# Optimization experiments

Hardware: AMD Instinct MI355X
Metric: run time of the kernel (lower is better)

Reference implementation:

```python
import jax, jax.numpy as jnp
import numpy as np

B, N, H, HEADS, L, V, T = 4, 256, 256, 4, 128, 256, 100
FF = 4 * H

def _ln(x, g, b, eps=1e-5):
    m = jnp.mean(x, -1, keepdims=True)
    v = jnp.mean((x - m) ** 2, -1, keepdims=True)
    return (x - m) / jnp.sqrt(v + eps) * g + b

def _mha(h, w_qkv, b_qkv, w_o, b_o):
    b, n, hd = h.shape
    d = hd // HEADS
    q, k, v = jnp.split(h @ w_qkv + b_qkv, 3, axis=-1)
    q = q.reshape(b, n, HEADS, d)
    k = k.reshape(b, n, HEADS, d)
    v = v.reshape(b, n, HEADS, d)
    s = jnp.einsum('bihd,bjhd->bhij', q, k) / jnp.sqrt(jnp.float32(d))
    a = jax.nn.softmax(s, axis=-1)
    o = jnp.einsum('bhij,bjhd->bihd', a, v).reshape(b, n, hd)
    return o @ w_o + b_o

def _edge_logits(h, w1, b1, w2, b2):
    # concat([h_i, h_j], -1) @ w1 == h_i @ w1[:H] + h_j @ w1[H:]  (avoids (B,N,N,2H) materialization)
    hi = h @ w1[:H]
    hj = h @ w1[H:]
    pre = hi[:, :, None, :] + hj[:, None, :, :] + b1  # (B,N,N,H)
    return (jax.nn.gelu(pre, approximate=False) @ w2 + b2)[..., 0]

def _gnn_block(x, nbr, qw, qb, kw, kb, vw, vb, sw, sb, l1g, l1b, f1w, f1b, f2w, f2b, l2g, l2b):
    # TransformerConv (PyG, concat=True, root_weight=True) as dense masked attention over in-neighbors.
    b, n, hd = x.shape
    d = hd // HEADS
    q = (x @ qw + qb).reshape(b, n, HEADS, d)
    k = (x @ kw + kb).reshape(b, n, HEADS, d)
    v = (x @ vw + vb).reshape(b, n, HEADS, d)
    s = jnp.einsum('bihd,bjhd->bhij', q, k) / jnp.sqrt(jnp.float32(d))
    m = nbr[:, None, :, :]  # (B,1,N,N); nbr[b,i,j]=True iff edge j->i
    a = jax.nn.softmax(jnp.where(m, s, -1e30), axis=-1) * m  # no-neighbor rows aggregate to 0
    agg = jnp.einsum('bhij,bjhd->bihd', a, v).reshape(b, n, hd)
    x = _ln(x + agg + x @ sw + sb, l1g, l1b)
    ffn = jax.nn.gelu(x @ f1w + f1b, approximate=False) @ f2w + f2b
    return _ln(x + ffn, l2g, l2b)

def _forward(noisy_tokens, t, z, lp1_w, lp1_b, lp2_w, lp2_b, tok_emb, time_tab, time_w, time_b, pos_tab, enc_qkv_w, enc_qkv_b, enc_o_w, enc_o_b, enc_ln1_g, enc_ln1_b, enc_f1_w, enc_f1_b, enc_f2_w, enc_f2_b, enc_ln2_g, enc_ln2_b, gq_w, gq_b, gk_w, gk_b, gv_w, gv_b, gs_w, gs_b, g_ln1_g, g_ln1_b, g_f1_w, g_f1_b, g_f2_w, g_f2_b, g_ln2_g, g_ln2_b, nh1_w, nh1_b, nh2_w, nh2_b, eh1_w, eh1_b, eh2_w, eh2_b, sh1_w, sh1_b, sh2_w, sh2_b):
    lat = jax.nn.relu(z @ lp1_w + lp1_b) @ lp2_w + lp2_b  # (B,H)
    time_e = jax.nn.gelu(time_tab[t] @ time_w + time_b, approximate=False)  # (B,H)
    h = tok_emb[noisy_tokens] + time_e[:, None, :] + pos_tab[None, :, :] + lat[:, None, :]
    for l in range(2):  # post-norm TransformerEncoderLayer, relu FFN
        h = _ln(h + _mha(h, enc_qkv_w[l], enc_qkv_b[l], enc_o_w[l], enc_o_b[l]), enc_ln1_g[l], enc_ln1_b[l])
        h = _ln(h + jax.nn.relu(h @ enc_f1_w[l] + enc_f1_b[l]) @ enc_f2_w[l] + enc_f2_b[l], enc_ln2_g[l], enc_ln2_b[l])
    el0 = _edge_logits(h, eh1_w, eh1_b, eh2_w, eh2_b)
    nbr = jnp.swapaxes(jax.nn.sigmoid(el0) > 0.3, 1, 2)  # transpose: adj[j,i] -> in-neighbors of i
    x = h
    for l in range(4):
        x = _gnn_block(x, nbr, gq_w[l], gq_b[l], gk_w[l], gk_b[l], gv_w[l], gv_b[l], gs_w[l], gs_b[l], g_ln1_g[l], g_ln1_b[l], g_f1_w[l], g_f1_b[l], g_f2_w[l], g_f2_b[l], g_ln2_g[l], g_ln2_b[l])
    node_logits = jax.nn.gelu(x @ nh1_w + nh1_b, approximate=False) @ nh2_w + nh2_b
    edge_logits = _edge_logits(x, eh1_w, eh1_b, eh2_w, eh2_b)
    size_logits = jax.nn.relu(lat @ sh1_w + sh1_b) @ sh2_w + sh2_b
    return node_logits, edge_logits, size_logits

def setup_inputs():
    key = jax.random.key(0)
    ks = iter(jax.random.split(key, 70))
    def p(shape):
        return jax.random.normal(next(ks), shape, dtype=jnp.float32) * 0.02
    return {
        'z': jax.random.normal(next(ks), (B, L), dtype=jnp.float32),
        'noisy_tokens': jax.random.randint(next(ks), (B, N), 0, V),
        't': jax.random.randint(next(ks), (B,), 0, T),
        'lp1_w': p((L, H)), 'lp1_b': p((H,)), 'lp2_w': p((H, H)), 'lp2_b': p((H,)),
        'tok_emb': p((V, H)), 'time_tab': p((T, H)), 'time_w': p((H, H)), 'time_b': p((H,)),
        'pos_tab': p((N, H)),
        'enc_qkv_w': p((2, H, 3 * H)), 'enc_qkv_b': p((2, 3 * H)),
        'enc_o_w': p((2, H, H)), 'enc_o_b': p((2, H)),
        'enc_ln1_g': jnp.ones((2, H)), 'enc_ln1_b': jnp.zeros((2, H)),
        'enc_f1_w': p((2, H, FF)), 'enc_f1_b': p((2, FF)),
        'enc_f2_w': p((2, FF, H)), 'enc_f2_b': p((2, H)),
        'enc_ln2_g': jnp.ones((2, H)), 'enc_ln2_b': jnp.zeros((2, H)),
        'gq_w': p((4, H, H)), 'gq_b': p((4, H)),
        'gk_w': p((4, H, H)), 'gk_b': p((4, H)),
        'gv_w': p((4, H, H)), 'gv_b': p((4, H)),
        'gs_w': p((4, H, H)), 'gs_b': p((4, H)),
        'g_ln1_g': jnp.ones((4, H)), 'g_ln1_b': jnp.zeros((4, H)),
        'g_f1_w': p((4, H, FF)), 'g_f1_b': p((4, FF)),
        'g_f2_w': p((4, FF, H)), 'g_f2_b': p((4, H)),
        'g_ln2_g': jnp.ones((4, H)), 'g_ln2_b': jnp.zeros((4, H)),
        'nh1_w': p((H, H)), 'nh1_b': p((H,)),
        'nh2_w': p((H, V)), 'nh2_b': p((V,)),
        'eh1_w': p((2 * H, H)), 'eh1_b': p((H,)),
        'eh2_w': p((H, 1)), 'eh2_b': p((1,)),
        'sh1_w': p((H, H // 2)), 'sh1_b': p((H // 2,)),
        'sh2_w': p((H // 2, N)), 'sh2_b': p((N,)),
    }

def reference(z, noisy_tokens, t, lp1_w, lp1_b, lp2_w, lp2_b, tok_emb, time_tab, time_w, time_b, pos_tab, enc_qkv_w, enc_qkv_b, enc_o_w, enc_o_b, enc_ln1_g, enc_ln1_b, enc_f1_w, enc_f1_b, enc_f2_w, enc_f2_b, enc_ln2_g, enc_ln2_b, gq_w, gq_b, gk_w, gk_b, gv_w, gv_b, gs_w, gs_b, g_ln1_g, g_ln1_b, g_f1_w, g_f1_b, g_f2_w, g_f2_b, g_ln2_g, g_ln2_b, nh1_w, nh1_b, nh2_w, nh2_b, eh1_w, eh1_b, eh2_w, eh2_b, sh1_w, sh1_b, sh2_w, sh2_b):
    return _forward(noisy_tokens, t, z, lp1_w, lp1_b, lp2_w, lp2_b, tok_emb, time_tab, time_w, time_b, pos_tab, enc_qkv_w, enc_qkv_b, enc_o_w, enc_o_b, enc_ln1_g, enc_ln1_b, enc_f1_w, enc_f1_b, enc_f2_w, enc_f2_b, enc_ln2_g, enc_ln2_b, gq_w, gq_b, gk_w, gk_b, gv_w, gv_b, gs_w, gs_b, g_ln1_g, g_ln1_b, g_f1_w, g_f1_b, g_f2_w, g_f2_b, g_ln2_g, g_ln2_b, nh1_w, nh1_b, nh2_w, nh2_b, eh1_w, eh1_b, eh2_w, eh2_b, sh1_w, sh1_b, sh2_w, sh2_b)
```

## Files before the change

kernel.cpp:

```cpp
#include <hip/hip_runtime.h>
#include <math.h>


typedef __attribute__((ext_vector_type(8))) short bf16x8;
typedef __attribute__((ext_vector_type(4))) float f32x4;

__device__ __forceinline__ unsigned short f2b(float f) {
    unsigned u = __float_as_uint(f);
    u += 0x7FFFu + ((u >> 16) & 1u);
    return (unsigned short)(u >> 16);
}
__device__ __forceinline__ unsigned pack2(float a, float b) {
    return (unsigned)f2b(a) | ((unsigned)f2b(b) << 16);
}
__device__ __forceinline__ bf16x8 as_frag(uint4 v) {
    union { uint4 u; bf16x8 f; } x; x.u = v; return x.f;
}
__device__ __forceinline__ bf16x8 ld_frag_f32(const float* p) {
    const float4 v0 = *(const float4*)p;
    const float4 v1 = *(const float4*)(p + 4);
    union { unsigned u[4]; bf16x8 f; } x;
    x.u[0] = pack2(v0.x, v0.y); x.u[1] = pack2(v0.z, v0.w);
    x.u[2] = pack2(v1.x, v1.y); x.u[3] = pack2(v1.z, v1.w);
    return x.f;
}

__device__ __forceinline__ float gelu_f(float x) {
    const float y  = 0.70710678118654752f * x;
    const float ay = fabsf(y);
    const float t  = __builtin_amdgcn_rcpf(fmaf(0.3275911f, ay, 1.0f));
    float S = fmaf(t, 1.061405429f, -1.453152027f);
    S = fmaf(t, S, 1.421413741f);
    S = fmaf(t, S, -0.284496736f);
    S = fmaf(t, S, 0.254829592f);
    S = S * t;
    const float e = __expf(-ay * ay);
    const float E = fmaf(-S, e, 1.0f);
    return 0.5f * x * (1.0f + copysignf(E, y));
}

struct PrepEnt { const float* src; unsigned dstOff; int K; int N; unsigned tstart; };
struct PrepTab { int n; PrepEnt e[36]; };

__global__ __launch_bounds__(256) void k_prep(PrepTab tab, unsigned short* __restrict__ wt)
{
    const int bx = blockIdx.x;
    int ei = 0;
    for (int i = 0; i < tab.n; ++i) if (tab.e[i].tstart <= (unsigned)bx) ei = i;
    const PrepEnt E = tab.e[ei];
    const int tIdx = bx - E.tstart;
    const int ntn = E.N >> 6;
    const int kt = tIdx / ntn, nt = tIdx % ntn;
    const int tid = threadIdx.x;
    __shared__ unsigned Tl[64][36];
    {
        const int r = tid >> 2, c = (tid & 3) * 16;
        const float* s = E.src + (size_t)(kt * 64 + r) * E.N + nt * 64 + c;
        unsigned o[8];
        #pragma unroll
        for (int q = 0; q < 4; ++q) {
            const float4 v = *(const float4*)(s + q * 4);
            o[q * 2 + 0] = pack2(v.x, v.y);
            o[q * 2 + 1] = pack2(v.z, v.w);
        }
        *(uint4*)&Tl[r][c / 2 + 0] = make_uint4(o[0], o[1], o[2], o[3]);
        *(uint4*)&Tl[r][c / 2 + 4] = make_uint4(o[4], o[5], o[6], o[7]);
    }
    __syncthreads();
    {
        const int rn = tid >> 2, ck = (tid & 3) * 16;
        const int sh = (rn & 1) * 16, hw = rn >> 1;
        unsigned o[8];
        #pragma unroll
        for (int s = 0; s < 8; ++s) {
            const unsigned lo = (Tl[ck + 2 * s][hw] >> sh) & 0xFFFFu;
            const unsigned hi = (Tl[ck + 2 * s + 1][hw] >> sh) & 0xFFFFu;
            o[s] = lo | (hi << 16);
        }
        unsigned short* d = wt + E.dstOff + (size_t)(nt * 64 + rn) * E.K + kt * 64 + ck;
        *(uint4*)(d + 0) = make_uint4(o[0], o[1], o[2], o[3]);
        *(uint4*)(d + 8) = make_uint4(o[4], o[5], o[6], o[7]);
    }
}


__device__ __forceinline__ void gd64_body(
    const float* __restrict__ A, const unsigned short* __restrict__ Wt,
    const float* __restrict__ bias, float* __restrict__ C,
    int K, int ldc, int act, int m0, int n0)
{
    const int tid = threadIdx.x;
    const int l = tid & 63, wid = tid >> 6;
    const int wm = wid & 1, wn = wid >> 1, lr = l & 15, lg = l >> 4;
    const float* a0 = A + (size_t)(m0 + wm * 32 + lr) * K + lg * 8;
    const float* a1 = a0 + (size_t)16 * K;
    const unsigned short* b0 = Wt + (size_t)(n0 + wn * 32 + lr) * K + lg * 8;
    const unsigned short* b1 = b0 + (size_t)16 * K;
    f32x4 acc00 = {0.f,0.f,0.f,0.f}, acc01 = acc00, acc10 = acc00, acc11 = acc00;
    #pragma unroll 2
    for (int k0 = 0; k0 < K; k0 += 32) {
        const bf16x8 fa0 = ld_frag_f32(a0 + k0);
        const bf16x8 fa1 = ld_frag_f32(a1 + k0);
        const bf16x8 fb0 = as_frag(*(const uint4*)(b0 + k0));
        const bf16x8 fb1 = as_frag(*(const uint4*)(b1 + k0));
        acc00 = __builtin_amdgcn_mfma_f32_16x16x32_bf16(fa0, fb0, acc00, 0, 0, 0);
        acc01 = __builtin_amdgcn_mfma_f32_16x16x32_bf16(fa0, fb1, acc01, 0, 0, 0);
        acc10 = __builtin_amdgcn_mfma_f32_16x16x32_bf16(fa1, fb0, acc10, 0, 0, 0);
        acc11 = __builtin_amdgcn_mfma_f32_16x16x32_bf16(fa1, fb1, acc11, 0, 0, 0);
    }
    const int cb0 = n0 + wn * 32 + lr, cb1 = cb0 + 16;
    const float bv0 = bias ? bias[cb0] : 0.f;
    const float bv1 = bias ? bias[cb1] : 0.f;
    #pragma unroll
    for (int r = 0; r < 4; ++r) {
        const int row0 = m0 + wm * 32 + lg * 4 + r;
        const int row1 = row0 + 16;
        float v00 = acc00[r] + bv0, v01 = acc01[r] + bv1;
        float v10 = acc10[r] + bv0, v11 = acc11[r] + bv1;
        if (act == 1) {
            v00 = fmaxf(v00, 0.f); v01 = fmaxf(v01, 0.f);
            v10 = fmaxf(v10, 0.f); v11 = fmaxf(v11, 0.f);
        } else if (act == 2) {
            v00 = gelu_f(v00); v01 = gelu_f(v01);
            v10 = gelu_f(v10); v11 = gelu_f(v11);
        }
        C[(size_t)row0 * ldc + cb0] = v00;
        C[(size_t)row0 * ldc + cb1] = v01;
        C[(size_t)row1 * ldc + cb0] = v10;
        C[(size_t)row1 * ldc + cb1] = v11;
    }
}

__global__ __launch_bounds__(256) void k_gd64(
    const float* __restrict__ A, const unsigned short* __restrict__ Wt,
    const float* __restrict__ bias, float* __restrict__ C, int K, int ldc, int act)
{
    gd64_body(A, Wt, bias, C, K, ldc, act, blockIdx.y * 64, blockIdx.x * 64);
}

__device__ __forceinline__ void gd32_body(
    const float* __restrict__ A, const unsigned short* __restrict__ Wt,
    const float* __restrict__ bias, float* __restrict__ C,
    int K, int ldc, int act, int m0, int n0)
{
    const int tid = threadIdx.x;
    const int l = tid & 63, wid = tid >> 6;
    const int qm = wid & 1, qn = wid >> 1, lr = l & 15, lg = l >> 4;
    const float* ap = A + (size_t)(m0 + qm * 16 + lr) * K + lg * 8;
    const unsigned short* bp = Wt + (size_t)(n0 + qn * 16 + lr) * K + lg * 8;
    f32x4 acc = {0.f,0.f,0.f,0.f};
    #pragma unroll 4
    for (int k0 = 0; k0 < K; k0 += 32) {
        const bf16x8 fa = ld_frag_f32(ap + k0);
        const bf16x8 fb = as_frag(*(const uint4*)(bp + k0));
        acc = __builtin_amdgcn_mfma_f32_16x16x32_bf16(fa, fb, acc, 0, 0, 0);
    }
    const int cc = n0 + qn * 16 + lr;
    const float bv = bias ? bias[cc] : 0.f;
    #pragma unroll
    for (int r = 0; r < 4; ++r) {
        const int row = m0 + qm * 16 + lg * 4 + r;
        float v = acc[r] + bv;
        if (act == 1) v = fmaxf(v, 0.f); else if (act == 2) v = gelu_f(v);
        C[(size_t)row * ldc + cc] = v;
    }
}

__global__ __launch_bounds__(256) void k_gd32(
    const float* __restrict__ A, const unsigned short* __restrict__ Wt,
    const float* __restrict__ bias, float* __restrict__ C, int K, int ldc, int act)
{
    gd32_body(A, Wt, bias, C, K, ldc, act, blockIdx.y * 32, blockIdx.x * 32);
}

struct MW4 { const unsigned short* wt[4]; const float* b[4]; };
__global__ __launch_bounds__(256) void k_gd32_4(
    const float* __restrict__ A, MW4 p, float* __restrict__ C)
{
    const int z = blockIdx.z;
    gd32_body(A, p.wt[z], p.b[z], C + z * 256, 256, 1024, 0,
              blockIdx.y * 32, blockIdx.x * 32);
}

__global__ __launch_bounds__(256) void k_mv(
    const float* __restrict__ A, const int* __restrict__ aidx, int K,
    const float* __restrict__ W, const float* __restrict__ bias,
    float* __restrict__ out, int N, int act)
{
    const int r = blockIdx.x, c0 = blockIdx.y * 64;
    const int c = threadIdx.x & 63, ks = threadIdx.x >> 6;
    const float* arow = A + (size_t)(aidx ? aidx[r] : r) * K;
    float s = 0.f;
    for (int k = ks; k < K; k += 4) s += arow[k] * W[(size_t)k * N + c0 + c];
    __shared__ float red[4][64];
    red[ks][c] = s;
    __syncthreads();
    if (ks == 0) {
        float v = red[0][c] + red[1][c] + red[2][c] + red[3][c] + (bias ? bias[c0 + c] : 0.f);
        if (act == 1) v = fmaxf(v, 0.f); else if (act == 2) v = gelu_f(v);
        out[(size_t)r * N + c0 + c] = v;
    }
}

__global__ __launch_bounds__(256) void k_embed(
    const int* __restrict__ tok, const float* __restrict__ tok_emb,
    const float* __restrict__ pos, const float* __restrict__ lat,
    const float* __restrict__ te, float* __restrict__ h)
{
    const int r = blockIdx.x, c = threadIdx.x;
    const int b = r >> 8, n = r & 255;
    h[(size_t)r * 256 + c] = tok_emb[(size_t)tok[r] * 256 + c] + te[b * 256 + c]
                           + pos[n * 256 + c] + lat[b * 256 + c];
}

__global__ __launch_bounds__(256) void k_attn2(
    const float* __restrict__ qkv, int ld, int qo, int ko, int vo,
    const unsigned char* __restrict__ mask, float* __restrict__ out)
{
    const int blk = blockIdx.x;
    const int ig = blk & 15, hh = (blk >> 4) & 3, b = blk >> 6;
    const int i0 = ig * 16;
    const int t = threadIdx.x;
    __shared__ float Qs[16][68];
    __shared__ float Ts[64][68];
    __shared__ float Ss[16][260];

    {
        const int r = t >> 4, c = (t & 15) * 4;
        *(float4*)&Qs[r][c] = *(const float4*)&qkv[(size_t)(b * 256 + i0 + r) * ld + qo + hh * 64 + c];
    }
    const int i = t >> 4, tx = t & 15;

    for (int jt = 0; jt < 4; ++jt) {
        __syncthreads();
        {
            const int jr = t >> 2, cs = (t & 3) * 16;
            const float* src = &qkv[(size_t)(b * 256 + jt * 64 + jr) * ld + ko + hh * 64 + cs];
            *(float4*)&Ts[jr][cs + 0]  = *(const float4*)(src + 0);
            *(float4*)&Ts[jr][cs + 4]  = *(const float4*)(src + 4);
            *(float4*)&Ts[jr][cs + 8]  = *(const float4*)(src + 8);
            *(float4*)&Ts[jr][cs + 12] = *(const float4*)(src + 12);
        }
        __syncthreads();
        float s0 = 0.f, s1 = 0.f, s2 = 0.f, s3 = 0.f;
        #pragma unroll 8
        for (int d = 0; d < 64; ++d) {
            const float qd = Qs[i][d];
            s0 += qd * Ts[tx][d];
            s1 += qd * Ts[tx + 16][d];
            s2 += qd * Ts[tx + 32][d];
            s3 += qd * Ts[tx + 48][d];
        }
        Ss[i][jt * 64 + tx]      = s0;
        Ss[i][jt * 64 + tx + 16] = s1;
        Ss[i][jt * 64 + tx + 32] = s2;
        Ss[i][jt * 64 + tx + 48] = s3;
    }

    {
        const unsigned char* mrow = mask ? &mask[(size_t)(b * 256 + i0 + i) * 256] : nullptr;
        float sv[16]; bool okv[16];
        float m = -3.0e38f;
        #pragma unroll
        for (int k = 0; k < 16; ++k) {
            const int j = tx + 16 * k;
            const float s = Ss[i][j] * 0.125f;
            const bool ok = mrow ? (mrow[j] != 0) : true;
            sv[k] = s; okv[k] = ok;
            if (ok) m = fmaxf(m, s);
        }
        #pragma unroll
        for (int w = 1; w < 16; w <<= 1) m = fmaxf(m, __shfl_xor(m, w, 64));
        float ev[16]; float sum = 0.f;
        #pragma unroll
        for (int k = 0; k < 16; ++k) {
            ev[k] = okv[k] ? __expf(sv[k] - m) : 0.f;
            sum += ev[k];
        }
        #pragma unroll
        for (int w = 1; w < 16; w <<= 1) sum += __shfl_xor(sum, w, 64);
        const float inv = (sum > 0.f) ? 1.f / sum : 0.f;
        #pragma unroll
        for (int k = 0; k < 16; ++k) Ss[i][tx + 16 * k] = ev[k] * inv;
    }

    const int d4 = tx * 4;
    float4 o = {0.f, 0.f, 0.f, 0.f};
    for (int jt = 0; jt < 4; ++jt) {
        __syncthreads();
        {
            const int jr = t >> 2, cs = (t & 3) * 16;
            const float* src = &qkv[(size_t)(b * 256 + jt * 64 + jr) * ld + vo + hh * 64 + cs];
            *(float4*)&Ts[jr][cs + 0]  = *(const float4*)(src + 0);
            *(float4*)&Ts[jr][cs + 4]  = *(const float4*)(src + 4);
            *(float4*)&Ts[jr][cs + 8]  = *(const float4*)(src + 8);
            *(float4*)&Ts[jr][cs + 12] = *(const float4*)(src + 12);
        }
        __syncthreads();
        #pragma unroll 8
        for (int j = 0; j < 64; ++j) {
            const float p = Ss[i][jt * 64 + j];
            const float4 v4 = *(const float4*)&Ts[j][d4];
            o.x += p * v4.x; o.y += p * v4.y; o.z += p * v4.z; o.w += p * v4.w;
        }
    }
    *(float4*)&out[(size_t)(b * 256 + i0 + i) * 256 + hh * 64 + d4] = o;
}

__global__ __launch_bounds__(256) void k_ln2(
    const float* __restrict__ a, const float* __restrict__ bb, int ldb,
    const float* __restrict__ cc, int ldc,
    const float* __restrict__ g, const float* __restrict__ beta, float* __restrict__ out)
{
    const int r = blockIdx.x * 4 + (threadIdx.x >> 6);
    const int c4 = (threadIdx.x & 63) * 4;
    float4 v = *(const float4*)&a[(size_t)r * 256 + c4];
    if (bb) {
        const float4 u = *(const float4*)&bb[(size_t)r * ldb + c4];
        v.x += u.x; v.y += u.y; v.z += u.z; v.w += u.w;
    }
    if (cc) {
        const float4 u = *(const float4*)&cc[(size_t)r * ldc + c4];
        v.x += u.x; v.y += u.y; v.z += u.z; v.w += u.w;
    }
    float s = v.x + v.y + v.z + v.w;
    float q = v.x * v.x + v.y * v.y + v.z * v.z + v.w * v.w;
    #pragma unroll
    for (int w = 1; w < 64; w <<= 1) {
        s += __shfl_xor(s, w, 64);
        q += __shfl_xor(q, w, 64);
    }
    const float mean = s * (1.0f / 256.0f);
    const float var  = q * (1.0f / 256.0f) - mean * mean;
    const float inv  = rsqrtf(var + 1e-5f);
    const float4 gg = *(const float4*)&g[c4];
    const float4 be = *(const float4*)&beta[c4];
    float4 o;
    o.x = (v.x - mean) * inv * gg.x + be.x;
    o.y = (v.y - mean) * inv * gg.y + be.y;
    o.z = (v.z - mean) * inv * gg.z + be.z;
    o.w = (v.w - mean) * inv * gg.w + be.w;
    *(float4*)&out[(size_t)r * 256 + c4] = o;
}

__global__ __launch_bounds__(256) void k_edge3(
    const float* __restrict__ hi, const float* __restrict__ hj,
    const float* __restrict__ w2, const float* __restrict__ b2,
    float* __restrict__ val_out, unsigned char* __restrict__ mask_out)
{
    const int jg = blockIdx.x, ig = blockIdx.y, b = blockIdx.z;
    const int t = threadIdx.x;
    __shared__ float his[16][268];
    __shared__ float hjs[16][268];
    __shared__ float w2s[256];
    {
        const int r = t >> 4, c = (t & 15) * 16;
        const float* s1 = &hi[(size_t)(b * 256 + ig * 16 + r) * 256 + c];
        const float* s2 = &hj[(size_t)(b * 256 + jg * 16 + r) * 256 + c];
        #pragma unroll
        for (int q = 0; q < 4; ++q) {
            *(float4*)&his[r][c + q * 4] = *(const float4*)(s1 + q * 4);
            *(float4*)&hjs[r][c + q * 4] = *(const float4*)(s2 + q * 4);
        }
        w2s[t] = w2[t];
    }
    __syncthreads();
    const int i = t >> 4, j = t & 15;
    float acc = 0.f;
    #pragma unroll 4
    for (int h4 = 0; h4 < 64; ++h4) {
        const float4 hv  = *(const float4*)&hjs[j][h4 * 4];
        const float4 hi4 = *(const float4*)&his[i][h4 * 4];
        const float4 w4  = *(const float4*)&w2s[h4 * 4];
        acc += gelu_f(hi4.x + hv.x) * w4.x;
        acc += gelu_f(hi4.y + hv.y) * w4.y;
        acc += gelu_f(hi4.z + hv.z) * w4.z;
        acc += gelu_f(hi4.w + hv.w) * w4.w;
    }
    const float v = acc + b2[0];
    if (val_out)  val_out[(size_t)b * 65536 + (ig * 16 + i) * 256 + jg * 16 + j] = v;
    if (mask_out) mask_out[(size_t)b * 65536 + (jg * 16 + j) * 256 + ig * 16 + i] =
                      (v > -0.84729786038720f) ? 1 : 0;
}

extern "C" void kernel_launch(void* const* d_in, const int* in_sizes, int n_in,
                              void* d_out, int out_size, void* d_ws, size_t ws_size,
                              hipStream_t stream) {
    const float* z     = (const float*)d_in[0];
    const int*   tok   = (const int*)d_in[1];
    const int*   tt    = (const int*)d_in[2];
    const float* lp1w  = (const float*)d_in[3];
    const float* lp1b  = (const float*)d_in[4];
    const float* lp2w  = (const float*)d_in[5];
    const float* lp2b  = (const float*)d_in[6];
    const float* temb  = (const float*)d_in[7];
    const float* ttab  = (const float*)d_in[8];
    const float* tw    = (const float*)d_in[9];
    const float* tb    = (const float*)d_in[10];
    const float* pos   = (const float*)d_in[11];
    const float* qkvw  = (const float*)d_in[12];
    const float* qkvb  = (const float*)d_in[13];
    const float* ow    = (const float*)d_in[14];
    const float* ob    = (const float*)d_in[15];
    const float* ln1g  = (const float*)d_in[16];
    const float* ln1b  = (const float*)d_in[17];
    const float* f1w   = (const float*)d_in[18];
    const float* f1b   = (const float*)d_in[19];
    const float* f2w   = (const float*)d_in[20];
    const float* f2b   = (const float*)d_in[21];
    const float* ln2g  = (const float*)d_in[22];
    const float* ln2b  = (const float*)d_in[23];
    const float* gqw   = (const float*)d_in[24];
    const float* gqb   = (const float*)d_in[25];
    const float* gkw   = (const float*)d_in[26];
    const float* gkb   = (const float*)d_in[27];
    const float* gvw   = (const float*)d_in[28];
    const float* gvb   = (const float*)d_in[29];
    const float* gsw   = (const float*)d_in[30];
    const float* gsb   = (const float*)d_in[31];
    const float* gl1g  = (const float*)d_in[32];
    const float* gl1b  = (const float*)d_in[33];
    const float* gf1w  = (const float*)d_in[34];
    const float* gf1b  = (const float*)d_in[35];
    const float* gf2w  = (const float*)d_in[36];
    const float* gf2b  = (const float*)d_in[37];
    const float* gl2g  = (const float*)d_in[38];
    const float* gl2b  = (const float*)d_in[39];
    const float* nh1w  = (const float*)d_in[40];
    const float* nh1b  = (const float*)d_in[41];
    const float* nh2w  = (const float*)d_in[42];
    const float* nh2b  = (const float*)d_in[43];
    const float* eh1w  = (const float*)d_in[44];
    const float* eh1b  = (const float*)d_in[45];
    const float* eh2w  = (const float*)d_in[46];
    const float* eh2b  = (const float*)d_in[47];
    const float* sh1w  = (const float*)d_in[48];
    const float* sh1b  = (const float*)d_in[49];
    const float* sh2w  = (const float*)d_in[50];
    const float* sh2b  = (const float*)d_in[51];

    float* W = (float*)d_ws;
    float* Hh  = W + 0;
    float* QK  = W + 262144;
    float* AO  = W + 1310720;
    float* T1  = W + 1572864;
    float* HI  = W + 1835008;
    float* HJ  = W + 2097152;
    float* LAT = W + 2359296;
    float* TE  = W + 2360320;
    float* A1  = W + 2361344;
    float* SH  = W + 2362368;
    unsigned char* MASK = (unsigned char*)(W + 2362880);
    unsigned short* wt  = (unsigned short*)(W + 2428416);

    float* out      = (float*)d_out;
    float* out_node = out;
    float* out_edge = out + 262144;
    float* out_sz   = out + 524288;

    PrepTab tab; int ne = 0; unsigned tiles = 0;
    auto add = [&](const float* src, int K, int N, unsigned off) {
        tab.e[ne].src = src; tab.e[ne].K = K; tab.e[ne].N = N;
        tab.e[ne].dstOff = off; tab.e[ne].tstart = tiles;
        tiles += (unsigned)((K >> 6) * (N >> 6)); ++ne;
    };
    for (int l = 0; l < 2; ++l) add(qkvw + (size_t)l * 196608, 256, 768,  0 + l * 196608);
    for (int l = 0; l < 2; ++l) add(ow   + (size_t)l * 65536,  256, 256,  393216 + l * 65536);
    for (int l = 0; l < 2; ++l) add(f1w  + (size_t)l * 262144, 256, 1024, 524288 + l * 262144);
    for (int l = 0; l < 2; ++l) add(f2w  + (size_t)l * 262144, 1024, 256, 1048576 + l * 262144);
    for (int l = 0; l < 4; ++l) add(gqw  + (size_t)l * 65536,  256, 256,  1572864 + l * 65536);
    for (int l = 0; l < 4; ++l) add(gkw  + (size_t)l * 65536,  256, 256,  1835008 + l * 65536);
    for (int l = 0; l < 4; ++l) add(gvw  + (size_t)l * 65536,  256, 256,  2097152 + l * 65536);
    for (int l = 0; l < 4; ++l) add(gsw  + (size_t)l * 65536,  256, 256,  2359296 + l * 65536);
    for (int l = 0; l < 4; ++l) add(gf1w + (size_t)l * 262144, 256, 1024, 2621440 + l * 262144);
    for (int l = 0; l < 4; ++l) add(gf2w + (size_t)l * 262144, 1024, 256, 3670016 + l * 262144);
    add(nh1w, 256, 256, 4718592);
    add(nh2w, 256, 256, 4784128);
    add(eh1w,         256, 256, 4849664);
    add(eh1w + 65536, 256, 256, 4915200);
    tab.n = ne;
    k_prep<<<tiles, 256, 0, stream>>>(tab, wt);

    auto g64 = [&](const float* Aa, size_t wtoff, const float* bias, float* Cc,
                   int N, int K, int ldc, int act) {
        k_gd64<<<dim3(N / 64, 16), 256, 0, stream>>>(Aa, wt + wtoff, bias, Cc, K, ldc, act);
    };
    auto g32 = [&](const float* Aa, size_t wtoff, const float* bias, float* Cc,
                   int K, int ldc, int act) {
        k_gd32<<<dim3(8, 32), 256, 0, stream>>>(Aa, wt + wtoff, bias, Cc, K, ldc, act);
    };

    k_mv<<<dim3(4, 4), 256, 0, stream>>>(z,    nullptr, 128, lp1w, lp1b, A1,     256, 1);
    k_mv<<<dim3(4, 4), 256, 0, stream>>>(ttab, tt,      256, tw,   tb,   TE,     256, 2);
    k_mv<<<dim3(4, 4), 256, 0, stream>>>(A1,   nullptr, 256, lp2w, lp2b, LAT,    256, 0);
    k_mv<<<dim3(4, 2), 256, 0, stream>>>(LAT,  nullptr, 256, sh1w, sh1b, SH,     128, 1);
    k_mv<<<dim3(4, 4), 256, 0, stream>>>(SH,   nullptr, 128, sh2w, sh2b, out_sz, 256, 0);

    k_embed<<<1024, 256, 0, stream>>>(tok, temb, pos, LAT, TE, Hh);

    for (int l = 0; l < 2; ++l) {
        g64(Hh, (size_t)l * 196608, qkvb + l * 768, QK, 768, 256, 768, 0);
        k_attn2<<<256, 256, 0, stream>>>(QK, 768, 0, 256, 512, nullptr, AO);
        g32(AO, 393216 + (size_t)l * 65536, ob + l * 256, T1, 256, 256, 0);
        k_ln2<<<256, 256, 0, stream>>>(Hh, T1, 256, nullptr, 0, ln1g + l * 256, ln1b + l * 256, Hh);
        g64(Hh, 524288 + (size_t)l * 262144, f1b + l * 1024, QK, 1024, 256, 1024, 1);
        g32(QK, 1048576 + (size_t)l * 262144, f2b + l * 256, T1, 1024, 256, 0);
        k_ln2<<<256, 256, 0, stream>>>(Hh, T1, 256, nullptr, 0, ln2g + l * 256, ln2b + l * 256, Hh);
    }

    g32(Hh, 4849664, eh1b, HI, 256, 256, 0);
    g32(Hh, 4915200, nullptr, HJ, 256, 256, 0);
    k_edge3<<<dim3(16, 16, 4), 256, 0, stream>>>(HI, HJ, eh2w, eh2b, nullptr, MASK);

    for (int l = 0; l < 4; ++l) {
        MW4 p;
        p.wt[0] = wt + 1572864 + (size_t)l * 65536; p.b[0] = gqb + l * 256;
        p.wt[1] = wt + 1835008 + (size_t)l * 65536; p.b[1] = gkb + l * 256;
        p.wt[2] = wt + 2097152 + (size_t)l * 65536; p.b[2] = gvb + l * 256;
        p.wt[3] = wt + 2359296 + (size_t)l * 65536; p.b[3] = gsb + l * 256;
        k_gd32_4<<<dim3(8, 32, 4), 256, 0, stream>>>(Hh, p, QK);
        k_attn2<<<256, 256, 0, stream>>>(QK, 1024, 0, 256, 512, MASK, AO);
        k_ln2<<<256, 256, 0, stream>>>(Hh, AO, 256, QK + 768, 1024, gl1g + l * 256, gl1b + l * 256, Hh);
        g64(Hh, 2621440 + (size_t)l * 262144, gf1b + l * 1024, QK, 1024, 256, 1024, 2);
        g32(QK, 3670016 + (size_t)l * 262144, gf2b + l * 256, T1, 1024, 256, 0);
        k_ln2<<<256, 256, 0, stream>>>(Hh, T1, 256, nullptr, 0, gl2g + l * 256, gl2b + l * 256, Hh);
    }

    g32(Hh, 4718592, nh1b, T1, 256, 256, 2);
    g32(T1, 4784128, nh2b, out_node, 256, 256, 0);
    g32(Hh, 4849664, eh1b, HI, 256, 256, 0);
    g32(Hh, 4915200, nullptr, HJ, 256, 256, 0);
    k_edge3<<<dim3(16, 16, 4), 256, 0, stream>>>(HI, HJ, eh2w, eh2b, out_edge, nullptr);
}
```

Baseline: 750.0 us.

## Fuse entire forward pass into one persistent kernel with grid barriers

```diff
diff --git a/kernel.cpp b/kernel.cpp
--- a/kernel.cpp
+++ b/kernel.cpp
@@ -1,6 +1,7 @@
 #include <hip/hip_runtime.h>
 #include <math.h>
 
+#define NB 256
 
 typedef __attribute__((ext_vector_type(8))) short bf16x8;
 typedef __attribute__((ext_vector_type(4))) float f32x4;
@@ -42,17 +43,46 @@
 struct PrepEnt { const float* src; unsigned dstOff; int K; int N; unsigned tstart; };
 struct PrepTab { int n; PrepEnt e[36]; };
 
-__global__ __launch_bounds__(256) void k_prep(PrepTab tab, unsigned short* __restrict__ wt)
-{
-    const int bx = blockIdx.x;
+struct MegaArgs {
+    const float *z; const int *tok; const int *tt;
+    const float *lp1w,*lp1b,*lp2w,*lp2b,*temb,*ttab,*tw,*tb,*pos;
+    const float *qkvb,*ob,*ln1g,*ln1b,*f1b,*f2b,*ln2g,*ln2b;
+    const float *gqb,*gkb,*gvb,*gsb,*gl1g,*gl1b,*gf1b,*gf2b,*gl2g,*gl2b;
+    const float *nh1b,*nh2b,*eh1b,*eh2w,*eh2b;
+    const float *sh1w,*sh1b,*sh2w,*sh2b;
+    float *Hh,*QK,*AO,*T1,*HI,*HJ,*LAT,*TE,*A1,*SH;
+    unsigned char* MASK; unsigned short* wt; unsigned* bar;
+    float *out_node,*out_edge,*out_sz;
+    PrepTab ptab;
+};
+
+__device__ __forceinline__ void gsync(unsigned* bar) {
+    __syncthreads();
+    if (threadIdx.x == 0) {
+        __threadfence();
+        unsigned g = __hip_atomic_load(bar + 1, __ATOMIC_RELAXED, __HIP_MEMORY_SCOPE_AGENT);
+        unsigned a = __hip_atomic_fetch_add(bar, 1u, __ATOMIC_ACQ_REL, __HIP_MEMORY_SCOPE_AGENT);
+        if (a == (unsigned)(NB - 1)) {
+            __hip_atomic_store(bar, 0u, __ATOMIC_RELAXED, __HIP_MEMORY_SCOPE_AGENT);
+            __hip_atomic_fetch_add(bar + 1, 1u, __ATOMIC_ACQ_REL, __HIP_MEMORY_SCOPE_AGENT);
+        } else {
+            while (__hip_atomic_load(bar + 1, __ATOMIC_ACQUIRE, __HIP_MEMORY_SCOPE_AGENT) == g)
+                __builtin_amdgcn_s_sleep(4);
+        }
+    }
+    __syncthreads();
+}
+
+__device__ void prep_tile(const PrepTab& tab, unsigned short* wt, int t, char* SMc)
+{
+    unsigned (*Tl)[36] = (unsigned(*)[36])SMc;
     int ei = 0;
-    for (int i = 0; i < tab.n; ++i) if (tab.e[i].tstart <= (unsigned)bx) ei = i;
+    for (int i = 0; i < tab.n; ++i) if (tab.e[i].tstart <= (unsigned)t) ei = i;
     const PrepEnt E = tab.e[ei];
-    const int tIdx = bx - E.tstart;
+    const int tIdx = t - (int)E.tstart;
     const int ntn = E.N >> 6;
     const int kt = tIdx / ntn, nt = tIdx % ntn;
     const int tid = threadIdx.x;
-    __shared__ unsigned Tl[64][36];
     {
         const int r = tid >> 2, c = (tid & 3) * 16;
         const float* s = E.src + (size_t)(kt * 64 + r) * E.N + nt * 64 + c;
@@ -81,67 +111,11 @@
         *(uint4*)(d + 0) = make_uint4(o[0], o[1], o[2], o[3]);
         *(uint4*)(d + 8) = make_uint4(o[4], o[5], o[6], o[7]);
     }
-}
-
-
-__device__ __forceinline__ void gd64_body(
-    const float* __restrict__ A, const unsigned short* __restrict__ Wt,
-    const float* __restrict__ bias, float* __restrict__ C,
-    int K, int ldc, int act, int m0, int n0)
-{
-    const int tid = threadIdx.x;
-    const int l = tid & 63, wid = tid >> 6;
-    const int wm = wid & 1, wn = wid >> 1, lr = l & 15, lg = l >> 4;
-    const float* a0 = A + (size_t)(m0 + wm * 32 + lr) * K + lg * 8;
-    const float* a1 = a0 + (size_t)16 * K;
-    const unsigned short* b0 = Wt + (size_t)(n0 + wn * 32 + lr) * K + lg * 8;
-    const unsigned short* b1 = b0 + (size_t)16 * K;
-    f32x4 acc00 = {0.f,0.f,0.f,0.f}, acc01 = acc00, acc10 = acc00, acc11 = acc00;
-    #pragma unroll 2
-    for (int k0 = 0; k0 < K; k0 += 32) {
-        const bf16x8 fa0 = ld_frag_f32(a0 + k0);
-        const bf16x8 fa1 = ld_frag_f32(a1 + k0);
-        const bf16x8 fb0 = as_frag(*(const uint4*)(b0 + k0));
-        const bf16x8 fb1 = as_frag(*(const uint4*)(b1 + k0));
-        acc00 = __builtin_amdgcn_mfma_f32_16x16x32_bf16(fa0, fb0, acc00, 0, 0, 0);
-        acc01 = __builtin_amdgcn_mfma_f32_16x16x32_bf16(fa0, fb1, acc01, 0, 0, 0);
-        acc10 = __builtin_amdgcn_mfma_f32_16x16x32_bf16(fa1, fb0, acc10, 0, 0, 0);
-        acc11 = __builtin_amdgcn_mfma_f32_16x16x32_bf16(fa1, fb1, acc11, 0, 0, 0);
-    }
-    const int cb0 = n0 + wn * 32 + lr, cb1 = cb0 + 16;
-    const float bv0 = bias ? bias[cb0] : 0.f;
-    const float bv1 = bias ? bias[cb1] : 0.f;
-    #pragma unroll
-    for (int r = 0; r < 4; ++r) {
-        const int row0 = m0 + wm * 32 + lg * 4 + r;
-        const int row1 = row0 + 16;
-        float v00 = acc00[r] + bv0, v01 = acc01[r] + bv1;
-        float v10 = acc10[r] + bv0, v11 = acc11[r] + bv1;
-        if (act == 1) {
-            v00 = fmaxf(v00, 0.f); v01 = fmaxf(v01, 0.f);
-            v10 = fmaxf(v10, 0.f); v11 = fmaxf(v11, 0.f);
-        } else if (act == 2) {
-            v00 = gelu_f(v00); v01 = gelu_f(v01);
-            v10 = gelu_f(v10); v11 = gelu_f(v11);
-        }
-        C[(size_t)row0 * ldc + cb0] = v00;
-        C[(size_t)row0 * ldc + cb1] = v01;
-        C[(size_t)row1 * ldc + cb0] = v10;
-        C[(size_t)row1 * ldc + cb1] = v11;
-    }
-}
-
-__global__ __launch_bounds__(256) void k_gd64(
-    const float* __restrict__ A, const unsigned short* __restrict__ Wt,
-    const float* __restrict__ bias, float* __restrict__ C, int K, int ldc, int act)
-{
-    gd64_body(A, Wt, bias, C, K, ldc, act, blockIdx.y * 64, blockIdx.x * 64);
-}
-
-__device__ __forceinline__ void gd32_body(
-    const float* __restrict__ A, const unsigned short* __restrict__ Wt,
-    const float* __restrict__ bias, float* __restrict__ C,
-    int K, int ldc, int act, int m0, int n0)
+    __syncthreads();
+}
+
+__device__ void gd32_tile(const float* A, const unsigned short* Wt, const float* bias,
+                          float* C, int K, int ldc, int act, int m0, int n0)
 {
     const int tid = threadIdx.x;
     const int l = tid & 63, wid = tid >> 6;
@@ -166,71 +140,20 @@
     }
 }
 
-__global__ __launch_bounds__(256) void k_gd32(
-    const float* __restrict__ A, const unsigned short* __restrict__ Wt,
-    const float* __restrict__ bias, float* __restrict__ C, int K, int ldc, int act)
-{
-    gd32_body(A, Wt, bias, C, K, ldc, act, blockIdx.y * 32, blockIdx.x * 32);
-}
-
-struct MW4 { const unsigned short* wt[4]; const float* b[4]; };
-__global__ __launch_bounds__(256) void k_gd32_4(
-    const float* __restrict__ A, MW4 p, float* __restrict__ C)
-{
-    const int z = blockIdx.z;
-    gd32_body(A, p.wt[z], p.b[z], C + z * 256, 256, 1024, 0,
-              blockIdx.y * 32, blockIdx.x * 32);
-}
-
-__global__ __launch_bounds__(256) void k_mv(
-    const float* __restrict__ A, const int* __restrict__ aidx, int K,
-    const float* __restrict__ W, const float* __restrict__ bias,
-    float* __restrict__ out, int N, int act)
-{
-    const int r = blockIdx.x, c0 = blockIdx.y * 64;
-    const int c = threadIdx.x & 63, ks = threadIdx.x >> 6;
-    const float* arow = A + (size_t)(aidx ? aidx[r] : r) * K;
-    float s = 0.f;
-    for (int k = ks; k < K; k += 4) s += arow[k] * W[(size_t)k * N + c0 + c];
-    __shared__ float red[4][64];
-    red[ks][c] = s;
-    __syncthreads();
-    if (ks == 0) {
-        float v = red[0][c] + red[1][c] + red[2][c] + red[3][c] + (bias ? bias[c0 + c] : 0.f);
-        if (act == 1) v = fmaxf(v, 0.f); else if (act == 2) v = gelu_f(v);
-        out[(size_t)r * N + c0 + c] = v;
-    }
-}
-
-__global__ __launch_bounds__(256) void k_embed(
-    const int* __restrict__ tok, const float* __restrict__ tok_emb,
-    const float* __restrict__ pos, const float* __restrict__ lat,
-    const float* __restrict__ te, float* __restrict__ h)
-{
-    const int r = blockIdx.x, c = threadIdx.x;
-    const int b = r >> 8, n = r & 255;
-    h[(size_t)r * 256 + c] = tok_emb[(size_t)tok[r] * 256 + c] + te[b * 256 + c]
-                           + pos[n * 256 + c] + lat[b * 256 + c];
-}
-
-__global__ __launch_bounds__(256) void k_attn2(
-    const float* __restrict__ qkv, int ld, int qo, int ko, int vo,
-    const unsigned char* __restrict__ mask, float* __restrict__ out)
-{
-    const int blk = blockIdx.x;
+__device__ void attn_block(const float* qkv, int ld, int qo, int ko, int vo,
+    const unsigned char* mask, float* outp, int blk, char* SMc)
+{
+    float (*Qs)[68]  = (float(*)[68])SMc;
+    float (*Ts)[68]  = (float(*)[68])(SMc + 4352);
+    float (*Ss)[260] = (float(*)[260])(SMc + 21760);
     const int ig = blk & 15, hh = (blk >> 4) & 3, b = blk >> 6;
     const int i0 = ig * 16;
     const int t = threadIdx.x;
-    __shared__ float Qs[16][68];
-    __shared__ float Ts[64][68];
-    __shared__ float Ss[16][260];
-
     {
         const int r = t >> 4, c = (t & 15) * 4;
         *(float4*)&Qs[r][c] = *(const float4*)&qkv[(size_t)(b * 256 + i0 + r) * ld + qo + hh * 64 + c];
     }
     const int i = t >> 4, tx = t & 15;
-
     for (int jt = 0; jt < 4; ++jt) {
         __syncthreads();
         {
@@ -256,7 +179,6 @@
         Ss[i][jt * 64 + tx + 32] = s2;
         Ss[i][jt * 64 + tx + 48] = s3;
     }
-
     {
         const unsigned char* mrow = mask ? &mask[(size_t)(b * 256 + i0 + i) * 256] : nullptr;
         float sv[16]; bool okv[16];
@@ -271,19 +193,18 @@
         }
         #pragma unroll
         for (int w = 1; w < 16; w <<= 1) m = fmaxf(m, __shfl_xor(m, w, 64));
-        float ev[16]; float sum = 0.f;
+        float sum = 0.f;
         #pragma unroll
         for (int k = 0; k < 16; ++k) {
-            ev[k] = okv[k] ? __expf(sv[k] - m) : 0.f;
-            sum += ev[k];
+            sv[k] = okv[k] ? __expf(sv[k] - m) : 0.f;
+            sum += sv[k];
         }
         #pragma unroll
         for (int w = 1; w < 16; w <<= 1) sum += __shfl_xor(sum, w, 64);
         const float inv = (sum > 0.f) ? 1.f / sum : 0.f;
         #pragma unroll
-        for (int k = 0; k < 16; ++k) Ss[i][tx + 16 * k] = ev[k] * inv;
-    }
-
+        for (int k = 0; k < 16; ++k) Ss[i][tx + 16 * k] = sv[k] * inv;
+    }
     const int d4 = tx * 4;
     float4 o = {0.f, 0.f, 0.f, 0.f};
     for (int jt = 0; jt < 4; ++jt) {
@@ -304,15 +225,14 @@
             o.x += p * v4.x; o.y += p * v4.y; o.z += p * v4.z; o.w += p * v4.w;
         }
     }
-    *(float4*)&out[(size_t)(b * 256 + i0 + i) * 256 + hh * 64 + d4] = o;
-}
-
-__global__ __launch_bounds__(256) void k_ln2(
-    const float* __restrict__ a, const float* __restrict__ bb, int ldb,
-    const float* __restrict__ cc, int ldc,
-    const float* __restrict__ g, const float* __restrict__ beta, float* __restrict__ out)
-{
-    const int r = blockIdx.x * 4 + (threadIdx.x >> 6);
+    *(float4*)&outp[(size_t)(b * 256 + i0 + i) * 256 + hh * 64 + d4] = o;
+    __syncthreads();
+}
+
+__device__ void ln_rows(const float* a, const float* bb, int ldb,
+    const float* cc, int ldc, const float* g, const float* beta, float* outp, int bid)
+{
+    const int r = bid * 4 + (threadIdx.x >> 6);
     const int c4 = (threadIdx.x & 63) * 4;
     float4 v = *(const float4*)&a[(size_t)r * 256 + c4];
     if (bb) {
@@ -340,19 +260,17 @@
     o.y = (v.y - mean) * inv * gg.y + be.y;
     o.z = (v.z - mean) * inv * gg.z + be.z;
     o.w = (v.w - mean) * inv * gg.w + be.w;
-    *(float4*)&out[(size_t)r * 256 + c4] = o;
-}
-
-__global__ __launch_bounds__(256) void k_edge3(
-    const float* __restrict__ hi, const float* __restrict__ hj,
-    const float* __restrict__ w2, const float* __restrict__ b2,
-    float* __restrict__ val_out, unsigned char* __restrict__ mask_out)
-{
-    const int jg = blockIdx.x, ig = blockIdx.y, b = blockIdx.z;
+    *(float4*)&outp[(size_t)r * 256 + c4] = o;
+}
+
+__device__ void edge_tile(const float* hi, const float* hj, const float* w2,
+    const float* b2, float* val_out, unsigned char* mask_out,
+    int b, int ig, int jg, char* SMc)
+{
+    float (*his)[268] = (float(*)[268])SMc;
+    float (*hjs)[268] = (float(*)[268])(SMc + 17152);
+    float* w2s = (float*)(SMc + 34304);
     const int t = threadIdx.x;
-    __shared__ float his[16][268];
-    __shared__ float hjs[16][268];
-    __shared__ float w2s[256];
     {
         const int r = t >> 4, c = (t & 15) * 16;
         const float* s1 = &hi[(size_t)(b * 256 + ig * 16 + r) * 256 + c];
@@ -381,6 +299,126 @@
     if (val_out)  val_out[(size_t)b * 65536 + (ig * 16 + i) * 256 + jg * 16 + j] = v;
     if (mask_out) mask_out[(size_t)b * 65536 + (jg * 16 + j) * 256 + ig * 16 + i] =
                       (v > -0.84729786038720f) ? 1 : 0;
+    __syncthreads();
+}
+
+__device__ void mv_chunk(const float* A, const int* aidx, int K, const float* Wm,
+                         const float* bias, float* outp, int N, int act,
+                         int rb, int cb, char* SMc)
+{
+    float (*red)[64] = (float(*)[64])SMc;
+    const int c = threadIdx.x & 63, ks = threadIdx.x >> 6;
+    const int c0 = cb * 64;
+    const float* arow = A + (size_t)(aidx ? aidx[rb] : rb) * K;
+    float s = 0.f;
+    for (int k = ks; k < K; k += 4) s += arow[k] * Wm[(size_t)k * N + c0 + c];
+    __syncthreads();
+    red[ks][c] = s;
+    __syncthreads();
+    if (ks == 0) {
+        float v = red[0][c] + red[1][c] + red[2][c] + red[3][c]
+                + (bias ? bias[c0 + c] : 0.f);
+        if (act == 1) v = fmaxf(v, 0.f); else if (act == 2) v = gelu_f(v);
+        outp[(size_t)rb * N + c0 + c] = v;
+    }
+}
+
+__global__ __launch_bounds__(256) void k_mega(MegaArgs A)
+{
+    __shared__ __align__(16) char SM[38912];
+    const int bid = blockIdx.x;
+    const int tid = threadIdx.x;
+
+    for (int t = bid; t < 1216; t += NB) prep_tile(A.ptab, A.wt, t, SM);
+    gsync(A.bar);
+
+    if (bid < 16) mv_chunk(A.z, nullptr, 128, A.lp1w, A.lp1b, A.A1, 256, 1, bid >> 2, bid & 3, SM);
+    else if (bid < 32) { const int b2 = bid - 16;
+        mv_chunk(A.ttab, A.tt, 256, A.tw, A.tb, A.TE, 256, 2, b2 >> 2, b2 & 3, SM); }
+    gsync(A.bar);
+
+    if (bid < 16) mv_chunk(A.A1, nullptr, 256, A.lp2w, A.lp2b, A.LAT, 256, 0, bid >> 2, bid & 3, SM);
+    gsync(A.bar);
+
+    for (int q = 0; q < 4; ++q) {
+        const int r = bid * 4 + q, b = r >> 8, n = r & 255;
+        A.Hh[(size_t)r * 256 + tid] = A.temb[(size_t)A.tok[r] * 256 + tid] + A.TE[b * 256 + tid]
+                                    + A.pos[n * 256 + tid] + A.LAT[b * 256 + tid];
+    }
+    if (bid < 8) mv_chunk(A.LAT, nullptr, 256, A.sh1w, A.sh1b, A.SH, 128, 1, bid >> 1, bid & 1, SM);
+    gsync(A.bar);
+
+    for (int l = 0; l < 2; ++l) {
+        for (int t = bid; t < 768; t += NB)
+            gd32_tile(A.Hh, A.wt + (size_t)l * 196608, A.qkvb + l * 768, A.QK,
+                      256, 768, 0, (t & 31) * 32, (t >> 5) * 32);
+        if (l == 0 && bid < 16)
+            mv_chunk(A.SH, nullptr, 128, A.sh2w, A.sh2b, A.out_sz, 256, 0, bid >> 2, bid & 3, SM);
+        gsync(A.bar);
+        attn_block(A.QK, 768, 0, 256, 512, nullptr, A.AO, bid, SM);
+        gsync(A.bar);
+        gd32_tile(A.AO, A.wt + 393216 + (size_t)l * 65536, A.ob + l * 256, A.T1,
+                  256, 256, 0, (bid & 31) * 32, (bid >> 5) * 32);
+        gsync(A.bar);
+        ln_rows(A.Hh, A.T1, 256, nullptr, 0, A.ln1g + l * 256, A.ln1b + l * 256, A.Hh, bid);
+        gsync(A.bar);
+        for (int t = bid; t < 1024; t += NB)
+            gd32_tile(A.Hh, A.wt + 524288 + (size_t)l * 262144, A.f1b + l * 1024, A.QK,
+                      256, 1024, 1, (t & 31) * 32, (t >> 5) * 32);
+        gsync(A.bar);
+        gd32_tile(A.QK, A.wt + 1048576 + (size_t)l * 262144, A.f2b + l * 256, A.T1,
+                  1024, 256, 0, (bid & 31) * 32, (bid >> 5) * 32);
+        gsync(A.bar);
+        ln_rows(A.Hh, A.T1, 256, nullptr, 0, A.ln2g + l * 256, A.ln2b + l * 256, A.Hh, bid);
+        gsync(A.bar);
+    }
+
+    for (int t = bid; t < 512; t += NB) {
+        const int s = t & 255, tm = (s & 31) * 32, tn = (s >> 5) * 32;
+        if (t < 256) gd32_tile(A.Hh, A.wt + 4849664, A.eh1b, A.HI, 256, 256, 0, tm, tn);
+        else         gd32_tile(A.Hh, A.wt + 4915200, nullptr, A.HJ, 256, 256, 0, tm, tn);
+    }
+    gsync(A.bar);
+    for (int t = bid; t < 1024; t += NB)
+        edge_tile(A.HI, A.HJ, A.eh2w, A.eh2b, nullptr, A.MASK, t >> 8, (t >> 4) & 15, t & 15, SM);
+    gsync(A.bar);
+
+    for (int l = 0; l < 4; ++l) {
+        for (int t = bid; t < 1024; t += NB) {
+            const int which = t >> 8, s = t & 255;
+            const unsigned short* w = A.wt + 1572864 + (size_t)which * 262144 + (size_t)l * 65536;
+            const float* bi = (which == 0 ? A.gqb : which == 1 ? A.gkb :
+                               which == 2 ? A.gvb : A.gsb) + l * 256;
+            gd32_tile(A.Hh, w, bi, A.QK + which * 256, 256, 1024, 0,
+                      (s & 31) * 32, (s >> 5) * 32);
+        }
+        gsync(A.bar);
+        attn_block(A.QK, 1024, 0, 256, 512, A.MASK, A.AO, bid, SM);
+        gsync(A.bar);
+        ln_rows(A.Hh, A.AO, 256, A.QK + 768, 1024, A.gl1g + l * 256, A.gl1b + l * 256, A.Hh, bid);
+        gsync(A.bar);
+        for (int t = bid; t < 1024; t += NB)
+            gd32_tile(A.Hh, A.wt + 2621440 + (size_t)l * 262144, A.gf1b + l * 1024, A.QK,
+                      256, 1024, 2, (t & 31) * 32, (t >> 5) * 32);
+        gsync(A.bar);
+        gd32_tile(A.QK, A.wt + 3670016 + (size_t)l * 262144, A.gf2b + l * 256, A.T1,
+                  1024, 256, 0, (bid & 31) * 32, (bid >> 5) * 32);
+        gsync(A.bar);
+        ln_rows(A.Hh, A.T1, 256, nullptr, 0, A.gl2g + l * 256, A.gl2b + l * 256, A.Hh, bid);
+        gsync(A.bar);
+    }
+
+    for (int t = bid; t < 768; t += NB) {
+        const int which = t >> 8, s = t & 255, tm = (s & 31) * 32, tn = (s >> 5) * 32;
+        if (which == 0)      gd32_tile(A.Hh, A.wt + 4718592, A.nh1b, A.T1, 256, 256, 2, tm, tn);
+        else if (which == 1) gd32_tile(A.Hh, A.wt + 4849664, A.eh1b, A.HI, 256, 256, 0, tm, tn);
+        else                 gd32_tile(A.Hh, A.wt + 4915200, nullptr, A.HJ, 256, 256, 0, tm, tn);
+    }
+    gsync(A.bar);
+    gd32_tile(A.T1, A.wt + 4784128, A.nh2b, A.out_node, 256, 256, 0,
+              (bid & 31) * 32, (bid >> 5) * 32);
+    for (int t = bid; t < 1024; t += NB)
+        edge_tile(A.HI, A.HJ, A.eh2w, A.eh2b, A.out_edge, nullptr, t >> 8, (t >> 4) & 15, t & 15, SM);
 }
 
 extern "C" void kernel_launch(void* const* d_in, const int* in_sizes, int n_in,
@@ -440,29 +478,34 @@
     const float* sh2b  = (const float*)d_in[51];
 
     float* W = (float*)d_ws;
-    float* Hh  = W + 0;
-    float* QK  = W + 262144;
-    float* AO  = W + 1310720;
-    float* T1  = W + 1572864;
-    float* HI  = W + 1835008;
-    float* HJ  = W + 2097152;
-    float* LAT = W + 2359296;
-    float* TE  = W + 2360320;
-    float* A1  = W + 2361344;
-    float* SH  = W + 2362368;
-    unsigned char* MASK = (unsigned char*)(W + 2362880);
-    unsigned short* wt  = (unsigned short*)(W + 2428416);
-
-    float* out      = (float*)d_out;
-    float* out_node = out;
-    float* out_edge = out + 262144;
-    float* out_sz   = out + 524288;
-
-    PrepTab tab; int ne = 0; unsigned tiles = 0;
+    MegaArgs A;
+    A.z = z; A.tok = tok; A.tt = tt;
+    A.lp1w = lp1w; A.lp1b = lp1b; A.lp2w = lp2w; A.lp2b = lp2b;
+    A.temb = temb; A.ttab = ttab; A.tw = tw; A.tb = tb; A.pos = pos;
+    A.qkvb = qkvb; A.ob = ob; A.ln1g = ln1g; A.ln1b = ln1b;
+    A.f1b = f1b; A.f2b = f2b; A.ln2g = ln2g; A.ln2b = ln2b;
+    A.gqb = gqb; A.gkb = gkb; A.gvb = gvb; A.gsb = gsb;
+    A.gl1g = gl1g; A.gl1b = gl1b; A.gf1b = gf1b; A.gf2b = gf2b;
+    A.gl2g = gl2g; A.gl2b = gl2b;
+    A.nh1b = nh1b; A.nh2b = nh2b; A.eh1b = eh1b; A.eh2w = eh2w; A.eh2b = eh2b;
+    A.sh1w = sh1w; A.sh1b = sh1b; A.sh2w = sh2w; A.sh2b = sh2b;
+
+    A.Hh = W + 0;           A.QK = W + 262144;     A.AO = W + 1310720;
+    A.T1 = W + 1572864;     A.HI = W + 1835008;    A.HJ = W + 2097152;
+    A.LAT = W + 2359296;    A.TE = W + 2360320;    A.A1 = W + 2361344;
+    A.SH = W + 2362368;
+    A.MASK = (unsigned char*)(W + 2362880);
+    A.wt   = (unsigned short*)(W + 2428416);
+    A.bar  = (unsigned*)(W + 4919296);
+
+    float* out = (float*)d_out;
+    A.out_node = out; A.out_edge = out + 262144; A.out_sz = out + 524288;
+
+    A.ptab.n = 0; unsigned tiles = 0;
     auto add = [&](const float* src, int K, int N, unsigned off) {
-        tab.e[ne].src = src; tab.e[ne].K = K; tab.e[ne].N = N;
-        tab.e[ne].dstOff = off; tab.e[ne].tstart = tiles;
-        tiles += (unsigned)((K >> 6) * (N >> 6)); ++ne;
+        PrepEnt& e = A.ptab.e[A.ptab.n++];
+        e.src = src; e.K = K; e.N = N; e.dstOff = off; e.tstart = tiles;
+        tiles += (unsigned)((K >> 6) * (N >> 6));
     };
     for (int l = 0; l < 2; ++l) add(qkvw + (size_t)l * 196608, 256, 768,  0 + l * 196608);
     for (int l = 0; l < 2; ++l) add(ow   + (size_t)l * 65536,  256, 256,  393216 + l * 65536);
@@ -478,57 +521,7 @@
     add(nh2w, 256, 256, 4784128);
     add(eh1w,         256, 256, 4849664);
     add(eh1w + 65536, 256, 256, 4915200);
-    tab.n = ne;
-    k_prep<<<tiles, 256, 0, stream>>>(tab, wt);
-
-    auto g64 = [&](const float* Aa, size_t wtoff, const float* bias, float* Cc,
-                   int N, int K, int ldc, int act) {
-        k_gd64<<<dim3(N / 64, 16), 256, 0, stream>>>(Aa, wt + wtoff, bias, Cc, K, ldc, act);
-    };
-    auto g32 = [&](const float* Aa, size_t wtoff, const float* bias, float* Cc,
-                   int K, int ldc, int act) {
-        k_gd32<<<dim3(8, 32), 256, 0, stream>>>(Aa, wt + wtoff, bias, Cc, K, ldc, act);
-    };
-
-    k_mv<<<dim3(4, 4), 256, 0, stream>>>(z,    nullptr, 128, lp1w, lp1b, A1,     256, 1);
-    k_mv<<<dim3(4, 4), 256, 0, stream>>>(ttab, tt,      256, tw,   tb,   TE,     256, 2);
-    k_mv<<<dim3(4, 4), 256, 0, stream>>>(A1,   nullptr, 256, lp2w, lp2b, LAT,    256, 0);
-    k_mv<<<dim3(4, 2), 256, 0, stream>>>(LAT,  nullptr, 256, sh1w, sh1b, SH,     128, 1);
-    k_mv<<<dim3(4, 4), 256, 0, stream>>>(SH,   nullptr, 128, sh2w, sh2b, out_sz, 256, 0);
-
-    k_embed<<<1024, 256, 0, stream>>>(tok, temb, pos, LAT, TE, Hh);
-
-    for (int l = 0; l < 2; ++l) {
-        g64(Hh, (size_t)l * 196608, qkvb + l * 768, QK, 768, 256, 768, 0);
-        k_attn2<<<256, 256, 0, stream>>>(QK, 768, 0, 256, 512, nullptr, AO);
-        g32(AO, 393216 + (size_t)l * 65536, ob + l * 256, T1, 256, 256, 0);
-        k_ln2<<<256, 256, 0, stream>>>(Hh, T1, 256, nullptr, 0, ln1g + l * 256, ln1b + l * 256, Hh);
-        g64(Hh, 524288 + (size_t)l * 262144, f1b + l * 1024, QK, 1024, 256, 1024, 1);
-        g32(QK, 1048576 + (size_t)l * 262144, f2b + l * 256, T1, 1024, 256, 0);
-        k_ln2<<<256, 256, 0, stream>>>(Hh, T1, 256, nullptr, 0, ln2g + l * 256, ln2b + l * 256, Hh);
-    }
-
-    g32(Hh, 4849664, eh1b, HI, 256, 256, 0);
-    g32(Hh, 4915200, nullptr, HJ, 256, 256, 0);
-    k_edge3<<<dim3(16, 16, 4), 256, 0, stream>>>(HI, HJ, eh2w, eh2b, nullptr, MASK);
-
-    for (int l = 0; l < 4; ++l) {
-        MW4 p;
-        p.wt[0] = wt + 1572864 + (size_t)l * 65536; p.b[0] = gqb + l * 256;
-        p.wt[1] = wt + 1835008 + (size_t)l * 65536; p.b[1] = gkb + l * 256;
-        p.wt[2] = wt + 2097152 + (size_t)l * 65536; p.b[2] = gvb + l * 256;
-        p.wt[3] = wt + 2359296 + (size_t)l * 65536; p.b[3] = gsb + l * 256;
-        k_gd32_4<<<dim3(8, 32, 4), 256, 0, stream>>>(Hh, p, QK);
-        k_attn2<<<256, 256, 0, stream>>>(QK, 1024, 0, 256, 512, MASK, AO);
-        k_ln2<<<256, 256, 0, stream>>>(Hh, AO, 256, QK + 768, 1024, gl1g + l * 256, gl1b + l * 256, Hh);
-        g64(Hh, 2621440 + (size_t)l * 262144, gf1b + l * 1024, QK, 1024, 256, 1024, 2);
-        g32(QK, 3670016 + (size_t)l * 262144, gf2b + l * 256, T1, 1024, 256, 0);
-        k_ln2<<<256, 256, 0, stream>>>(Hh, T1, 256, nullptr, 0, gl2g + l * 256, gl2b + l * 256, Hh);
-    }
-
-    g32(Hh, 4718592, nh1b, T1, 256, 256, 2);
-    g32(T1, 4784128, nh2b, out_node, 256, 256, 0);
-    g32(Hh, 4849664, eh1b, HI, 256, 256, 0);
-    g32(Hh, 4915200, nullptr, HJ, 256, 256, 0);
-    k_edge3<<<dim3(16, 16, 4), 256, 0, stream>>>(HI, HJ, eh2w, eh2b, out_edge, nullptr);
-}
+
+    hipMemsetAsync(A.bar, 0, 8, stream);
+    k_mega<<<NB, 256, 0, stream>>>(A);
+}
```

New measurement: 2.261 ms. 201% more time.
